# Kernel optimization log

Measured on AMD Instinct MI355X. Metric: run time of the kernel, lower is better.

Reference implementation:

```python
import jax, jax.numpy as jnp
import numpy as np

B, C, T = 32, 1536, 2000
BN_EPS = 1e-5


def setup_inputs() -> dict:
    key = jax.random.key(0)
    k1, k2 = jax.random.split(key)
    x = jax.random.normal(k1, (B, C, T), dtype=jnp.float32)
    conv_w = jax.random.normal(k2, (C,), dtype=jnp.float32) * (1.0 / np.sqrt(C))
    conv_b = jnp.zeros((1,), dtype=jnp.float32)
    bn_gamma = jnp.ones((1,), dtype=jnp.float32)
    bn_beta = jnp.zeros((1,), dtype=jnp.float32)
    return {"x": x, "conv_w": conv_w, "conv_b": conv_b,
            "bn_gamma": bn_gamma, "bn_beta": bn_beta}


def reference(x, conv_w, conv_b, bn_gamma, bn_beta):
    # attention conv: 1x1 Conv1d C->1  == per-frame dot product  -> [B, T]
    a = jnp.einsum('bct,c->bt', x, conv_w) + conv_b[0]
    # BatchNorm1d(1) in training mode: batch stats over (B, T), biased var
    mu = jnp.mean(a)
    var = jnp.mean((a - mu) ** 2)
    a = (a - mu) * jax.lax.rsqrt(var + BN_EPS) * bn_gamma[0] + bn_beta[0]
    # tanh + softmax over time
    attn = jax.nn.softmax(jnp.tanh(a), axis=1)          # [B, T]
    # weighted statistics pooling
    mean = jnp.einsum('bct,bt->bc', x, attn)             # [B, C]
    diff = x - mean[:, :, None]
    var_w = jnp.einsum('bct,bt->bc', diff * diff, attn)  # [B, C]
    std = jnp.sqrt(jnp.clip(var_w, 1e-10, None))
    return jnp.concatenate([mean, std], axis=1)          # [B, 2C]
```

## Files before the change

kernel.cpp:

```cpp
#include <hip/hip_runtime.h>
#include <math.h>

#define B 32
#define C 1536
#define T 2000
#define NBT (B * T)
#define CSPLIT 8
#define CCH (C / CSPLIT)
#define T4 (T / 4)
#define BN_EPS 1e-5f
#define K2_BLOCKS 250


__global__ __launch_bounds__(256) void k1_conv(const float* __restrict__ x,
                                               const float* __restrict__ w,
                                               float* __restrict__ a_part) {
  const int t4 = blockIdx.x * 256 + threadIdx.x;
  const int b  = blockIdx.y;
  const int ck = blockIdx.z;
  if (t4 >= T4) return;
  const int c0 = ck * CCH;
  const float4* xp = reinterpret_cast<const float4*>(x) + ((size_t)b * C + c0) * T4;
  float4 acc = make_float4(0.f, 0.f, 0.f, 0.f);
#pragma unroll 8
  for (int j = 0; j < CCH; ++j) {
    const float wc = w[c0 + j];
    const float4 v = xp[(size_t)j * T4 + t4];
    acc.x += v.x * wc; acc.y += v.y * wc; acc.z += v.z * wc; acc.w += v.w * wc;
  }
  reinterpret_cast<float4*>(a_part + (size_t)ck * NBT + b * T)[t4] = acc;
}

__global__ __launch_bounds__(256) void k2_reduce(const float* __restrict__ a_part,
                                                 const float* __restrict__ conv_b,
                                                 float* __restrict__ a,
                                                 float* __restrict__ psums) {
  const int i = blockIdx.x * 256 + threadIdx.x;
  float v = conv_b[0];
#pragma unroll
  for (int k = 0; k < CSPLIT; ++k) v += a_part[(size_t)k * NBT + i];
  a[i] = v;

  float s1 = v, s2 = v * v;
#pragma unroll
  for (int off = 32; off; off >>= 1) {
    s1 += __shfl_xor(s1, off);
    s2 += __shfl_xor(s2, off);
  }
  __shared__ float ls1[4], ls2[4];
  const int wid = threadIdx.x >> 6, lane = threadIdx.x & 63;
  if (lane == 0) { ls1[wid] = s1; ls2[wid] = s2; }
  __syncthreads();
  if (threadIdx.x == 0) {
    psums[blockIdx.x]             = ls1[0] + ls1[1] + ls1[2] + ls1[3];
    psums[K2_BLOCKS + blockIdx.x] = ls2[0] + ls2[1] + ls2[2] + ls2[3];
  }
}

__global__ __launch_bounds__(256) void k3_softmax(const float* __restrict__ a,
                                                  const float* __restrict__ psums,
                                                  const float* __restrict__ gamma,
                                                  const float* __restrict__ beta,
                                                  float* __restrict__ attn) {
  __shared__ float sv[T];
  __shared__ float r1[4], r2[4], r3[4], r4[4];
  const int tid = threadIdx.x;
  const int wid = tid >> 6, lane = tid & 63;

  float s1 = 0.f, s2 = 0.f;
  if (tid < K2_BLOCKS) { s1 = psums[tid]; s2 = psums[K2_BLOCKS + tid]; }
#pragma unroll
  for (int off = 32; off; off >>= 1) {
    s1 += __shfl_xor(s1, off);
    s2 += __shfl_xor(s2, off);
  }
  if (lane == 0) { r1[wid] = s1; r2[wid] = s2; }
  __syncthreads();
  const float tot1 = r1[0] + r1[1] + r1[2] + r1[3];
  const float tot2 = r2[0] + r2[1] + r2[2] + r2[3];
  const float mu  = tot1 / (float)NBT;
  const float var = tot2 / (float)NBT - mu * mu;
  const float rs  = 1.0f / sqrtf(var + BN_EPS);
  const float g = gamma[0], be = beta[0];

  const int b = blockIdx.x;
  const float* ab = a + b * T;
  float lmax = -1e30f;
  for (int t = tid; t < T; t += 256) {
    const float v = tanhf((ab[t] - mu) * rs * g + be);
    sv[t] = v;
    lmax = fmaxf(lmax, v);
  }
#pragma unroll
  for (int off = 32; off; off >>= 1) lmax = fmaxf(lmax, __shfl_xor(lmax, off));
  if (lane == 0) r3[wid] = lmax;
  __syncthreads();
  const float m = fmaxf(fmaxf(r3[0], r3[1]), fmaxf(r3[2], r3[3]));

  float lsum = 0.f;
  for (int t = tid; t < T; t += 256) {
    const float p = expf(sv[t] - m);
    sv[t] = p;
    lsum += p;
  }
#pragma unroll
  for (int off = 32; off; off >>= 1) lsum += __shfl_xor(lsum, off);
  if (lane == 0) r4[wid] = lsum;
  __syncthreads();
  const float inv = 1.0f / (r4[0] + r4[1] + r4[2] + r4[3]);

  for (int t = tid; t < T; t += 256) attn[b * T + t] = sv[t] * inv;
}

__global__ __launch_bounds__(256) void k4_pool(const float* __restrict__ x,
                                               const float* __restrict__ attn,
                                               float* __restrict__ out) {
  const int wid  = threadIdx.x >> 6;
  const int lane = threadIdx.x & 63;
  const int row  = blockIdx.x * 4 + wid;
  const int b = row / C;
  const int c = row - b * C;
  const float4* xr = reinterpret_cast<const float4*>(x)    + (size_t)row * T4;
  const float4* ar = reinterpret_cast<const float4*>(attn) + (size_t)b   * T4;
  float sxa = 0.f, sx2a = 0.f;
  for (int j = lane; j < T4; j += 64) {
    const float4 xv = xr[j];
    const float4 av = ar[j];
    sxa  += xv.x * av.x + xv.y * av.y + xv.z * av.z + xv.w * av.w;
    sx2a += xv.x * xv.x * av.x + xv.y * xv.y * av.y +
            xv.z * xv.z * av.z + xv.w * xv.w * av.w;
  }
#pragma unroll
  for (int off = 32; off; off >>= 1) {
    sxa  += __shfl_xor(sxa, off);
    sx2a += __shfl_xor(sx2a, off);
  }
  if (lane == 0) {
    const float mean = sxa;
    out[(size_t)b * 2 * C + c]     = mean;
    out[(size_t)b * 2 * C + C + c] = sqrtf(fmaxf(sx2a - mean * mean, 1e-10f));
  }
}

extern "C" void kernel_launch(void* const* d_in, const int* in_sizes, int n_in,
                              void* d_out, int out_size, void* d_ws, size_t ws_size,
                              hipStream_t stream) {
  const float* x      = (const float*)d_in[0];
  const float* conv_w = (const float*)d_in[1];
  const float* conv_b = (const float*)d_in[2];
  const float* gamma  = (const float*)d_in[3];
  const float* beta   = (const float*)d_in[4];
  float* out = (float*)d_out;

  float* ws     = (float*)d_ws;
  float* a_part = ws;
  float* a      = a_part + (size_t)CSPLIT * NBT;
  float* attn   = a + NBT;
  float* psums  = attn + NBT;

  dim3 g1((T4 + 255) / 256, B, CSPLIT);
  k1_conv<<<g1, 256, 0, stream>>>(x, conv_w, a_part);
  k2_reduce<<<K2_BLOCKS, 256, 0, stream>>>(a_part, conv_b, a, psums);
  k3_softmax<<<B, 256, 0, stream>>>(a, psums, gamma, beta, attn);
  k4_pool<<<(B * C) / 4, 256, 0, stream>>>(x, attn, out);
}
```

Before: 571.8 us.

## Split channels finer, widen softmax block, preload pooling rows with nontemporal loads

Doubles the channel split in the conv kernel so more blocks stream x, at the cost of twice the partial-sum traffic in the reduce kernel. Uses native vector types for the accumulation. The softmax kernel moves to 512 threads. The pooling kernel fully unrolls its row loop and issues all eight float4 loads up front with nontemporal hints, raising memory-level parallelism while adding register pressure.

```diff
diff --git a/kernel.cpp b/kernel.cpp
--- a/kernel.cpp
+++ b/kernel.cpp
@@ -5,11 +5,13 @@
 #define C 1536
 #define T 2000
 #define NBT (B * T)
-#define CSPLIT 8
+#define CSPLIT 16
 #define CCH (C / CSPLIT)
 #define T4 (T / 4)
 #define BN_EPS 1e-5f
 #define K2_BLOCKS 250
+
+using f4 = __attribute__((ext_vector_type(4))) float;
 
 
 __global__ __launch_bounds__(256) void k1_conv(const float* __restrict__ x,
@@ -20,15 +22,15 @@
   const int ck = blockIdx.z;
   if (t4 >= T4) return;
   const int c0 = ck * CCH;
-  const float4* xp = reinterpret_cast<const float4*>(x) + ((size_t)b * C + c0) * T4;
-  float4 acc = make_float4(0.f, 0.f, 0.f, 0.f);
+  const f4* xp = reinterpret_cast<const f4*>(x) + ((size_t)b * C + c0) * T4;
+  f4 acc = (f4)0.f;
 #pragma unroll 8
   for (int j = 0; j < CCH; ++j) {
     const float wc = w[c0 + j];
-    const float4 v = xp[(size_t)j * T4 + t4];
-    acc.x += v.x * wc; acc.y += v.y * wc; acc.z += v.z * wc; acc.w += v.w * wc;
+    const f4 v = xp[(size_t)j * T4 + t4];
+    acc += v * wc;
   }
-  reinterpret_cast<float4*>(a_part + (size_t)ck * NBT + b * T)[t4] = acc;
+  reinterpret_cast<f4*>(a_part + (size_t)ck * NBT + b * T)[t4] = acc;
 }
 
 __global__ __launch_bounds__(256) void k2_reduce(const float* __restrict__ a_part,
@@ -57,13 +59,13 @@
   }
 }
 
-__global__ __launch_bounds__(256) void k3_softmax(const float* __restrict__ a,
+__global__ __launch_bounds__(512) void k3_softmax(const float* __restrict__ a,
                                                   const float* __restrict__ psums,
                                                   const float* __restrict__ gamma,
                                                   const float* __restrict__ beta,
                                                   float* __restrict__ attn) {
   __shared__ float sv[T];
-  __shared__ float r1[4], r2[4], r3[4], r4[4];
+  __shared__ float r1[8], r2[8], r3[8], r4[8];
   const int tid = threadIdx.x;
   const int wid = tid >> 6, lane = tid & 63;
 
@@ -76,8 +78,9 @@
   }
   if (lane == 0) { r1[wid] = s1; r2[wid] = s2; }
   __syncthreads();
-  const float tot1 = r1[0] + r1[1] + r1[2] + r1[3];
-  const float tot2 = r2[0] + r2[1] + r2[2] + r2[3];
+  float tot1 = 0.f, tot2 = 0.f;
+#pragma unroll
+  for (int k = 0; k < 8; ++k) { tot1 += r1[k]; tot2 += r2[k]; }
   const float mu  = tot1 / (float)NBT;
   const float var = tot2 / (float)NBT - mu * mu;
   const float rs  = 1.0f / sqrtf(var + BN_EPS);
@@ -86,7 +89,7 @@
   const int b = blockIdx.x;
   const float* ab = a + b * T;
   float lmax = -1e30f;
-  for (int t = tid; t < T; t += 256) {
+  for (int t = tid; t < T; t += 512) {
     const float v = tanhf((ab[t] - mu) * rs * g + be);
     sv[t] = v;
     lmax = fmaxf(lmax, v);
@@ -95,10 +98,12 @@
   for (int off = 32; off; off >>= 1) lmax = fmaxf(lmax, __shfl_xor(lmax, off));
   if (lane == 0) r3[wid] = lmax;
   __syncthreads();
-  const float m = fmaxf(fmaxf(r3[0], r3[1]), fmaxf(r3[2], r3[3]));
+  float m = -1e30f;
+#pragma unroll
+  for (int k = 0; k < 8; ++k) m = fmaxf(m, r3[k]);
 
   float lsum = 0.f;
-  for (int t = tid; t < T; t += 256) {
+  for (int t = tid; t < T; t += 512) {
     const float p = expf(sv[t] - m);
     sv[t] = p;
     lsum += p;
@@ -107,9 +112,12 @@
   for (int off = 32; off; off >>= 1) lsum += __shfl_xor(lsum, off);
   if (lane == 0) r4[wid] = lsum;
   __syncthreads();
-  const float inv = 1.0f / (r4[0] + r4[1] + r4[2] + r4[3]);
+  float tot = 0.f;
+#pragma unroll
+  for (int k = 0; k < 8; ++k) tot += r4[k];
+  const float inv = 1.0f / tot;
 
-  for (int t = tid; t < T; t += 256) attn[b * T + t] = sv[t] * inv;
+  for (int t = tid; t < T; t += 512) attn[b * T + t] = sv[t] * inv;
 }
 
 __global__ __launch_bounds__(256) void k4_pool(const float* __restrict__ x,
@@ -120,15 +128,30 @@
   const int row  = blockIdx.x * 4 + wid;
   const int b = row / C;
   const int c = row - b * C;
-  const float4* xr = reinterpret_cast<const float4*>(x)    + (size_t)row * T4;
-  const float4* ar = reinterpret_cast<const float4*>(attn) + (size_t)b   * T4;
+  const f4* xr = reinterpret_cast<const f4*>(x)    + (size_t)row * T4;
+  const f4* ar = reinterpret_cast<const f4*>(attn) + (size_t)b   * T4;
+
+  f4 xv[8], av[8];
+#pragma unroll
+  for (int j = 0; j < 7; ++j) {
+    xv[j] = __builtin_nontemporal_load(xr + j * 64 + lane);
+    av[j] = ar[j * 64 + lane];
+  }
+  if (lane < 52) {
+    xv[7] = __builtin_nontemporal_load(xr + 448 + lane);
+    av[7] = ar[448 + lane];
+  } else {
+    xv[7] = (f4)0.f;
+    av[7] = (f4)0.f;
+  }
+
   float sxa = 0.f, sx2a = 0.f;
-  for (int j = lane; j < T4; j += 64) {
-    const float4 xv = xr[j];
-    const float4 av = ar[j];
-    sxa  += xv.x * av.x + xv.y * av.y + xv.z * av.z + xv.w * av.w;
-    sx2a += xv.x * xv.x * av.x + xv.y * xv.y * av.y +
-            xv.z * xv.z * av.z + xv.w * xv.w * av.w;
+#pragma unroll
+  for (int j = 0; j < 8; ++j) {
+    const f4 xa = xv[j] * av[j];
+    sxa  += xa.x + xa.y + xa.z + xa.w;
+    const f4 x2a = xv[j] * xa;
+    sx2a += x2a.x + x2a.y + x2a.z + x2a.w;
   }
 #pragma unroll
   for (int off = 32; off; off >>= 1) {
@@ -161,6 +184,6 @@
   dim3 g1((T4 + 255) / 256, B, CSPLIT);
   k1_conv<<<g1, 256, 0, stream>>>(x, conv_w, a_part);
   k2_reduce<<<K2_BLOCKS, 256, 0, stream>>>(a_part, conv_b, a, psums);
-  k3_softmax<<<B, 256, 0, stream>>>(a, psums, gamma, beta, attn);
+  k3_softmax<<<B, 512, 0, stream>>>(a, psums, gamma, beta, attn);
   k4_pool<<<(B * C) / 4, 256, 0, stream>>>(x, attn, out);
 }
```

New measurement: 561.3 us. Within noise of the previous version (-1.8%).
